# Performance work log

Hardware: AMD Instinct MI355X
Metric: run time of the kernel (lower is better)

The kernel has to match this reference:

```python
import jax, jax.numpy as jnp
import numpy as np

B, T, C, H = 4, 4096, 1024, 64

def setup_inputs() -> dict:
    key = jax.random.key(0)
    kx, kq, kk, kv = jax.random.split(key, 4)
    x = jax.random.normal(kx, (B, T, C), dtype=jnp.float32)
    scale = 1.0 / np.sqrt(C)
    Wq = jax.random.normal(kq, (C, H), dtype=jnp.float32) * scale
    Wk = jax.random.normal(kk, (C, H), dtype=jnp.float32) * scale
    Wv = jax.random.normal(kv, (C, H), dtype=jnp.float32) * scale
    return {"x": x, "Wq": Wq, "Wk": Wk, "Wv": Wv}

def reference(x, Wq, Wk, Wv):
    Bsz, Tlen, _ = x.shape
    head_size = Wq.shape[1]
    q = x @ Wq  # [B,T,H]
    k = x @ Wk
    v = x @ Wv
    # scores [B,T,T], scaled by sqrt(head_size)
    scores = jnp.einsum('bqh,bkh->bqk', q, k) / jnp.sqrt(jnp.float32(head_size))
    causal = jnp.tril(jnp.ones((Tlen, Tlen), dtype=bool))
    scores = jnp.where(causal, scores, -jnp.inf)
    weights = jax.nn.softmax(scores, axis=-1)
    # dropout p=0.0 -> identity
    return jnp.einsum('bqk,bkh->bqh', weights, v)
```

## Files before the change

### kernel.cpp

```cpp
#include <hip/hip_runtime.h>
#include <hip/hip_bf16.h>

typedef __attribute__((ext_vector_type(8))) short short8;
typedef __attribute__((ext_vector_type(4))) float f32x4;

#define MFMA16(a, b, c) __builtin_amdgcn_mfma_f32_16x16x32_bf16((a), (b), (c), 0, 0, 0)

typedef const __attribute__((address_space(1))) unsigned int* gas_t;
typedef __attribute__((address_space(3))) unsigned int* las_t;
#define GLDS16(g, l) __builtin_amdgcn_global_load_lds((gas_t)(g), (las_t)(l), 16, 0, 0)

__device__ inline unsigned short f2bf(float f) {
    union { float f; unsigned int u; } v;
    v.f = f;
    unsigned int u = v.u;
    return (unsigned short)((u + 0x7fffu + ((u >> 16) & 1u)) >> 16);
}

__device__ inline float bf2f(unsigned short u) {
    union { unsigned int u; float f; } v;
    v.u = ((unsigned int)u) << 16;
    return v.f;
}

__device__ inline size_t WF(int n, int c) {
    return ((((size_t)(n >> 4)) * 32 + (c >> 5)) * 64 + ((c >> 3) & 3) * 16 + (n & 15)) * 8 + (c & 7);
}
__device__ inline size_t QKF(int q, int h) {
    return ((((size_t)(q >> 4)) * 2 + (h >> 5)) * 64 + ((h >> 3) & 3) * 16 + (q & 15)) * 8 + (h & 7);
}
__device__ inline size_t VF(int h, int t) {
    return ((((size_t)(h >> 4)) * 128 + (t >> 5)) * 64 + ((t >> 3) & 3) * 16 + (h & 15)) * 8 + (t & 7);
}

__global__ __launch_bounds__(256) void prep_w(const float* __restrict__ Wq,
                                              const float* __restrict__ Wk,
                                              const float* __restrict__ Wv,
                                              unsigned short* __restrict__ Wt) {
    int idx = blockIdx.x * 256 + threadIdx.x;
    if (idx >= 192 * 1024) return;
    int n = idx >> 10;
    int c = idx & 1023;
    const float* W = (n < 64) ? Wq : ((n < 128) ? Wk : Wv);
    float v = W[c * 64 + (n & 63)];
    if (n < 64) v *= 0.125f;
    Wt[WF(n, c)] = f2bf(v);
}

__global__ __launch_bounds__(256, 4) void projt(const float* __restrict__ x,
                                                const unsigned short* __restrict__ Wt,
                                                unsigned short* __restrict__ Qs,
                                                unsigned short* __restrict__ Ks,
                                                unsigned short* __restrict__ Vt) {
    __shared__ __align__(16) float xbuf[2][32 * 128];

    const int tid = threadIdx.x;
    const int w = tid >> 6;
    const int lane = tid & 63;
    const int lr = lane & 15;
    const int lg = lane >> 4;
    const int t0 = blockIdx.x * 32;

    f32x4 acc[2][3];
#pragma unroll
    for (int rg = 0; rg < 2; rg++)
#pragma unroll
        for (int i = 0; i < 3; i++) acc[rg][i] = (f32x4){0.f, 0.f, 0.f, 0.f};

#define STAGE_X(buf, c0)                                                       \
    {                                                                          \
        _Pragma("unroll")                                                      \
        for (int p = 0; p < 4; p++) {                                          \
            int row = w * 8 + p * 2 + (lane >> 5);                             \
            int chunk = (lane & 31) ^ (row & 7);                               \
            const float* src = x + (size_t)(t0 + row) * 1024 + (c0) + chunk * 4;\
            float* dst = &xbuf[buf][(w * 8 + p * 2) * 128];  \
            GLDS16(src, dst);                                                  \
        }                                                                      \
    }

    STAGE_X(0, 0);
    __syncthreads();

    int cur = 0;
    for (int t = 0; t < 8; ++t) {
        if (t < 7) STAGE_X(cur ^ 1, (t + 1) * 128);

        const char* xb = (const char*)&xbuf[cur][0];
#pragma unroll
        for (int h = 0; h < 4; h++) {
            short8 bfr[3];
#pragma unroll
            for (int nt = 0; nt < 3; nt++)
                bfr[nt] = *(const short8*)(Wt +
                    (((size_t)(w * 3 + nt) * 32 + (t * 4 + h)) * 64 + lane) * 8);
            int cb = h * 8 + lg * 2;
            short8 a[2];
#pragma unroll
            for (int rg = 0; rg < 2; rg++) {
                int row = rg * 16 + lr;
                float4 a0 = *(const float4*)(xb + row * 512 + ((cb) ^ (row & 7)) * 16);
                float4 a1 = *(const float4*)(xb + row * 512 + ((cb + 1) ^ (row & 7)) * 16);
                short8 av;
                av[0] = (short)f2bf(a0.x); av[1] = (short)f2bf(a0.y);
                av[2] = (short)f2bf(a0.z); av[3] = (short)f2bf(a0.w);
                av[4] = (short)f2bf(a1.x); av[5] = (short)f2bf(a1.y);
                av[6] = (short)f2bf(a1.z); av[7] = (short)f2bf(a1.w);
                a[rg] = av;
            }
#pragma unroll
            for (int rg = 0; rg < 2; rg++)
#pragma unroll
                for (int nt = 0; nt < 3; nt++)
                    acc[rg][nt] = MFMA16(a[rg], bfr[nt], acc[rg][nt]);
        }
        __syncthreads();
        cur ^= 1;
    }

    const int nbase = w * 48;
#pragma unroll
    for (int rg = 0; rg < 2; rg++) {
#pragma unroll
        for (int nt = 0; nt < 3; nt++) {
#pragma unroll
            for (int r = 0; r < 4; r++) {
                int n = nbase + nt * 16 + lr;
                int tq = t0 + rg * 16 + lg * 4 + r;
                int b = tq >> 12;
                int qq = tq & 4095;
                unsigned short val = f2bf(acc[rg][nt][r]);
                if (n < 64) {
                    Qs[(size_t)b * 262144 + QKF(qq, n)] = val;
                } else if (n < 128) {
                    Ks[(size_t)b * 262144 + QKF(qq, n - 64)] = val;
                } else {
                    Vt[(size_t)b * 262144 + VF(n - 128, qq)] = val;
                }
            }
        }
    }
}

#define SROW 72

template <int NS>
__global__ __launch_bounds__(64) void attn(const unsigned short* __restrict__ Qs,
                                           const unsigned short* __restrict__ Ks,
                                           const unsigned short* __restrict__ Vt,
                                           float* __restrict__ out,
                                           unsigned short* __restrict__ accP,
                                           float* __restrict__ mP,
                                           float* __restrict__ lP) {
    __shared__ unsigned short pl[32 * SROW];

    const int ntasks = 512 * NS;
    int raw = ntasks - 1 - blockIdx.x;
    int qt_g = raw / NS;
    int c = raw - qt_g * NS;
    int qt = qt_g >> 2;
    int b = qt_g & 3;
    int q0 = qt * 32;

    int lane = threadIdx.x;
    int lr = lane & 15;
    int lg = lane >> 4;

    const unsigned short* Qb = Qs + (size_t)b * 262144;
    const unsigned short* Kb = Ks + (size_t)b * 262144;
    const unsigned short* Vb = Vt + (size_t)b * 262144;

    short8 qf[2][2];
#pragma unroll
    for (int qs = 0; qs < 2; qs++)
#pragma unroll
        for (int kh = 0; kh < 2; kh++)
            qf[qs][kh] = *(const short8*)(Qb +
                (((size_t)((q0 >> 4) + qs) * 2 + kh) * 64 + lane) * 8);

    f32x4 acc[4][2];
#pragma unroll
    for (int i = 0; i < 4; i++)
#pragma unroll
        for (int qs = 0; qs < 2; qs++) acc[i][qs] = (f32x4){0.f, 0.f, 0.f, 0.f};
    float m[2] = {-1e30f, -1e30f};
    float l[2] = {0.f, 0.f};

    int nt = (q0 + 95) >> 6;
    int tb = (c * nt) / NS;
    int te = ((c + 1) * nt) / NS;

    short8 kf[4][2];
    if (tb < te) {
#pragma unroll
        for (int t = 0; t < 4; t++)
#pragma unroll
            for (int half = 0; half < 2; half++)
                kf[t][half] = *(const short8*)(Kb +
                    (((size_t)((tb * 64) >> 4) + t) * 2 + half) * 512 + lane * 8);
    }

    for (int t64 = tb; t64 < te; ++t64) {
        int kv0 = t64 * 64;

        f32x4 s[4][2];
#pragma unroll
        for (int t = 0; t < 4; t++)
#pragma unroll
            for (int qs = 0; qs < 2; qs++) {
                f32x4 z = (f32x4){0.f, 0.f, 0.f, 0.f};
                z = MFMA16(kf[t][0], qf[qs][0], z);
                z = MFMA16(kf[t][1], qf[qs][1], z);
                s[t][qs] = z;
            }

        short8 vf[4][2];
#pragma unroll
        for (int ht = 0; ht < 4; ht++)
#pragma unroll
            for (int half = 0; half < 2; half++)
                vf[ht][half] = *(const short8*)(Vb +
                    (((size_t)ht * 128 + (kv0 >> 5) + half) * 64 + lane) * 8);

        if (t64 + 1 < te) {
            int kvn = (t64 + 1) * 64;
#pragma unroll
            for (int t = 0; t < 4; t++)
#pragma unroll
                for (int half = 0; half < 2; half++)
                    kf[t][half] = *(const short8*)(Kb +
                        (((size_t)(kvn >> 4) + t) * 2 + half) * 512 + lane * 8);
        }

        if (kv0 + 63 > q0) {
#pragma unroll
            for (int t = 0; t < 4; t++)
#pragma unroll
                for (int qs = 0; qs < 2; qs++)
#pragma unroll
                    for (int r = 0; r < 4; r++) {
                        int kv = kv0 + t * 16 + lg * 4 + r;
                        if (kv > q0 + qs * 16 + lr) s[t][qs][r] = -1e30f;
                    }
        }

        float pmax[2] = {-1e30f, -1e30f};
#pragma unroll
        for (int t = 0; t < 4; t++)
#pragma unroll
            for (int qs = 0; qs < 2; qs++)
#pragma unroll
                for (int r = 0; r < 4; r++) pmax[qs] = fmaxf(pmax[qs], s[t][qs][r]);

        int ok = (pmax[0] <= m[0] + 8.0f) && (pmax[1] <= m[1] + 8.0f);
        if (!__all(ok)) {
            float alpha[2];
#pragma unroll
            for (int qs = 0; qs < 2; qs++) {
                float mx = pmax[qs];
                mx = fmaxf(mx, __shfl_xor(mx, 16));
                mx = fmaxf(mx, __shfl_xor(mx, 32));
                float mn = fmaxf(m[qs], mx);
                alpha[qs] = __expf(m[qs] - mn);
                m[qs] = mn;
                l[qs] *= alpha[qs];
            }
            float ar[2][4];
#pragma unroll
            for (int qs = 0; qs < 2; qs++)
#pragma unroll
                for (int r = 0; r < 4; r++) ar[qs][r] = __shfl(alpha[qs], lg * 4 + r);
#pragma unroll
            for (int ht = 0; ht < 4; ht++)
#pragma unroll
                for (int qs = 0; qs < 2; qs++)
#pragma unroll
                    for (int r = 0; r < 4; r++) acc[ht][qs][r] *= ar[qs][r];
        }

#pragma unroll
        for (int t = 0; t < 4; t++)
#pragma unroll
            for (int qs = 0; qs < 2; qs++)
#pragma unroll
                for (int r = 0; r < 4; r++) {
                    float e = __expf(s[t][qs][r] - m[qs]);
                    s[t][qs][r] = e;
                    l[qs] += e;
                }

#pragma unroll
        for (int qs = 0; qs < 2; qs++)
#pragma unroll
            for (int t = 0; t < 4; t++) {
                uint2 uu;
                uu.x = (unsigned)f2bf(s[t][qs][0]) | ((unsigned)f2bf(s[t][qs][1]) << 16);
                uu.y = (unsigned)f2bf(s[t][qs][2]) | ((unsigned)f2bf(s[t][qs][3]) << 16);
                *(uint2*)&pl[(qs * 16 + lr) * SROW + t * 16 + lg * 4] = uu;
            }
        asm volatile("s_waitcnt lgkmcnt(0)" ::: "memory");
        __builtin_amdgcn_sched_barrier(0);
        short8 pa[2][2];
#pragma unroll
        for (int qs = 0; qs < 2; qs++)
#pragma unroll
            for (int half = 0; half < 2; half++)
                pa[qs][half] = *(const short8*)&pl[(qs * 16 + lr) * SROW +
                                                   half * 32 + lg * 8];

#pragma unroll
        for (int ht = 0; ht < 4; ht++)
#pragma unroll
            for (int qs = 0; qs < 2; qs++) {
                acc[ht][qs] = MFMA16(pa[qs][0], vf[ht][0], acc[ht][qs]);
                acc[ht][qs] = MFMA16(pa[qs][1], vf[ht][1], acc[ht][qs]);
            }
    }

    float lt[2];
#pragma unroll
    for (int qs = 0; qs < 2; qs++) {
        float v = l[qs];
        v += __shfl_xor(v, 16);
        v += __shfl_xor(v, 32);
        lt[qs] = v;
    }

    if (NS == 1) {
        float rl[2][4];
#pragma unroll
        for (int qs = 0; qs < 2; qs++)
#pragma unroll
            for (int r = 0; r < 4; r++) rl[qs][r] = 1.0f / __shfl(lt[qs], lg * 4 + r);
#pragma unroll
        for (int ht = 0; ht < 4; ht++)
#pragma unroll
            for (int qs = 0; qs < 2; qs++)
#pragma unroll
                for (int r = 0; r < 4; r++) {
                    size_t o = ((size_t)b * 4096 + q0 + qs * 16 + lg * 4 + r) * 64 +
                               ht * 16 + lr;
                    out[o] = acc[ht][qs][r] * rl[qs][r];
                }
    } else {
        int tidx = qt_g * NS + c;
        unsigned short* ap = accP + (size_t)tidx * 2048;
#pragma unroll
        for (int ht = 0; ht < 4; ht++)
#pragma unroll
            for (int qs = 0; qs < 2; qs++)
#pragma unroll
                for (int r = 0; r < 4; r++)
                    ap[(qs * 16 + lg * 4 + r) * 64 + ht * 16 + lr] =
                        f2bf(acc[ht][qs][r]);
        if (lane < 16) {
#pragma unroll
            for (int qs = 0; qs < 2; qs++) {
                mP[tidx * 32 + qs * 16 + lane] = m[qs];
                lP[tidx * 32 + qs * 16 + lane] = lt[qs];
            }
        }
    }
}

template <int NS>
__global__ __launch_bounds__(256) void combine(const unsigned short* __restrict__ accP,
                                               const float* __restrict__ mP,
                                               const float* __restrict__ lP,
                                               float* __restrict__ out) {
    int g = blockIdx.x * 256 + threadIdx.x;
    int h = g & 63;
    int row = g >> 6;
    int b = row >> 12;
    int t = row & 4095;
    int qt = t >> 5;
    int qr = t & 31;
    int qt_g = qt * 4 + b;

    float mc[NS];
    float M = -1e30f;
#pragma unroll
    for (int c = 0; c < NS; c++) {
        mc[c] = mP[(qt_g * NS + c) * 32 + qr];
        M = fmaxf(M, mc[c]);
    }
    float num = 0.f, den = 0.f;
#pragma unroll
    for (int c = 0; c < NS; c++) {
        float wgt = __expf(mc[c] - M);
        den += wgt * lP[(qt_g * NS + c) * 32 + qr];
        num += wgt * bf2f(accP[(size_t)(qt_g * NS + c) * 2048 + qr * 64 + h]);
    }
    out[g] = num / den;
}

extern "C" void kernel_launch(void* const* d_in, const int* in_sizes, int n_in,
                              void* d_out, int out_size, void* d_ws, size_t ws_size,
                              hipStream_t stream) {
    const float* x  = (const float*)d_in[0];
    const float* Wq = (const float*)d_in[1];
    const float* Wk = (const float*)d_in[2];
    const float* Wv = (const float*)d_in[3];
    float* out = (float*)d_out;

    char* ws = (char*)d_ws;
    unsigned short* Qs = (unsigned short*)(ws);
    unsigned short* Ks = (unsigned short*)(ws + (2u << 20));
    unsigned short* Vt = (unsigned short*)(ws + (4u << 20));
    unsigned short* Wt = (unsigned short*)(ws + (6u << 20));
    unsigned short* accP = (unsigned short*)(ws + (8u << 20));
    float* mP = (float*)(ws + (24u << 20));
    float* lP = (float*)(ws + (24u << 20) + (512u << 10));

    prep_w<<<768, 256, 0, stream>>>(Wq, Wk, Wv, Wt);
    projt<<<512, 256, 0, stream>>>(x, Wt, Qs, Ks, Vt);

    if (ws_size >= (25u << 20)) {
        attn<8><<<4096, 64, 0, stream>>>(Qs, Ks, Vt, out, accP, mP, lP);
        combine<8><<<4096, 256, 0, stream>>>(accP, mP, lP, out);
    } else {
        attn<1><<<512, 64, 0, stream>>>(Qs, Ks, Vt, out, accP, mP, lP);
    }
}
```

Measured before the change: 71.25 us.

## Register-prefetch x slabs in projection and halve attention KV split count

The projection kernel stops using async global-to-LDS loads. It now loads 64-column slabs of x into registers two steps ahead, writes them to a smaller double-buffered LDS tile with a new XOR swizzle, and uses a single barrier per step with a fully unrolled 16-step loop. Separately, the split-KV attention drops from 8 splits to 4, halving the attention grid and the partial results the combine kernel must merge. The trade-offs are more registers and less parallelism in attention.

```diff
diff --git a/kernel.cpp b/kernel.cpp
--- a/kernel.cpp
+++ b/kernel.cpp
@@ -5,10 +5,6 @@
 typedef __attribute__((ext_vector_type(4))) float f32x4;
 
 #define MFMA16(a, b, c) __builtin_amdgcn_mfma_f32_16x16x32_bf16((a), (b), (c), 0, 0, 0)
-
-typedef const __attribute__((address_space(1))) unsigned int* gas_t;
-typedef __attribute__((address_space(3))) unsigned int* las_t;
-#define GLDS16(g, l) __builtin_amdgcn_global_load_lds((gas_t)(g), (las_t)(l), 16, 0, 0)
 
 __device__ inline unsigned short f2bf(float f) {
     union { float f; unsigned int u; } v;
@@ -52,7 +48,7 @@
                                                 unsigned short* __restrict__ Qs,
                                                 unsigned short* __restrict__ Ks,
                                                 unsigned short* __restrict__ Vt) {
-    __shared__ __align__(16) float xbuf[2][32 * 128];
+    __shared__ __align__(16) float xbuf[2][32 * 64];
 
     const int tid = threadIdx.x;
     const int w = tid >> 6;
@@ -61,46 +57,65 @@
     const int lg = lane >> 4;
     const int t0 = blockIdx.x * 32;
 
-    f32x4 acc[2][3];
-#pragma unroll
-    for (int rg = 0; rg < 2; rg++)
-#pragma unroll
-        for (int i = 0; i < 3; i++) acc[rg][i] = (f32x4){0.f, 0.f, 0.f, 0.f};
-
-#define STAGE_X(buf, c0)                                                       \
+    const int sr0 = w * 8 + (lane >> 4);
+    const int sch = lane & 15;
+
+#define LOADSLAB(v, sl)                                                        \
+    {                                                                          \
+        const uint4* xr = (const uint4*)(x + (size_t)(t0) * 1024 + (sl) * 64); \
+        v[0] = xr[(size_t)(sr0) * 256 + sch];                                  \
+        v[1] = xr[(size_t)(sr0 + 4) * 256 + sch];                              \
+    }
+
+#define DSWRITE(buf, v)                                                        \
     {                                                                          \
         _Pragma("unroll")                                                      \
-        for (int p = 0; p < 4; p++) {                                          \
-            int row = w * 8 + p * 2 + (lane >> 5);                             \
-            int chunk = (lane & 31) ^ (row & 7);                               \
-            const float* src = x + (size_t)(t0 + row) * 1024 + (c0) + chunk * 4;\
-            float* dst = &xbuf[buf][(w * 8 + p * 2) * 128];  \
-            GLDS16(src, dst);                                                  \
+        for (int j = 0; j < 2; j++) {                                          \
+            int row = sr0 + j * 4;                                             \
+            int l = sch ^ (row & 15);                                          \
+            *(uint4*)&xbuf[buf][row * 64 + l * 4] = v[j];                      \
         }                                                                      \
     }
 
-    STAGE_X(0, 0);
-    __syncthreads();
-
-    int cur = 0;
-    for (int t = 0; t < 8; ++t) {
-        if (t < 7) STAGE_X(cur ^ 1, (t + 1) * 128);
-
-        const char* xb = (const char*)&xbuf[cur][0];
-#pragma unroll
-        for (int h = 0; h < 4; h++) {
+    uint4 vc[2], vn[2];
+    LOADSLAB(vc, 0);
+    DSWRITE(0, vc);
+    LOADSLAB(vc, 1);
+
+    f32x4 acc[2][3];
+#pragma unroll
+    for (int rg = 0; rg < 2; rg++)
+#pragma unroll
+        for (int i = 0; i < 3; i++) acc[rg][i] = (f32x4){0.f, 0.f, 0.f, 0.f};
+
+#pragma unroll
+    for (int t = 0; t < 16; ++t) {
+        if (t + 2 < 16) LOADSLAB(vn, t + 2);
+
+        asm volatile("s_waitcnt lgkmcnt(0)" ::: "memory");
+        __builtin_amdgcn_sched_barrier(0);
+        __builtin_amdgcn_s_barrier();
+        __builtin_amdgcn_sched_barrier(0);
+
+        if (t + 1 < 16) DSWRITE((t + 1) & 1, vc);
+
+        const float* xb = &xbuf[t & 1][0];
+#pragma unroll
+        for (int h = 0; h < 2; h++) {
             short8 bfr[3];
 #pragma unroll
             for (int nt = 0; nt < 3; nt++)
                 bfr[nt] = *(const short8*)(Wt +
-                    (((size_t)(w * 3 + nt) * 32 + (t * 4 + h)) * 64 + lane) * 8);
+                    (((size_t)(w * 3 + nt) * 32 + (t * 2 + h)) * 64 + lane) * 8);
             int cb = h * 8 + lg * 2;
+            int l0 = cb ^ lr;
+            int l1 = (cb + 1) ^ lr;
             short8 a[2];
 #pragma unroll
             for (int rg = 0; rg < 2; rg++) {
                 int row = rg * 16 + lr;
-                float4 a0 = *(const float4*)(xb + row * 512 + ((cb) ^ (row & 7)) * 16);
-                float4 a1 = *(const float4*)(xb + row * 512 + ((cb + 1) ^ (row & 7)) * 16);
+                float4 a0 = *(const float4*)&xb[row * 64 + l0 * 4];
+                float4 a1 = *(const float4*)&xb[row * 64 + l1 * 4];
                 short8 av;
                 av[0] = (short)f2bf(a0.x); av[1] = (short)f2bf(a0.y);
                 av[2] = (short)f2bf(a0.z); av[3] = (short)f2bf(a0.w);
@@ -114,8 +129,8 @@
                 for (int nt = 0; nt < 3; nt++)
                     acc[rg][nt] = MFMA16(a[rg], bfr[nt], acc[rg][nt]);
         }
-        __syncthreads();
-        cur ^= 1;
+
+        if (t + 2 < 16) { vc[0] = vn[0]; vc[1] = vn[1]; }
     }
 
     const int nbase = w * 48;
@@ -416,8 +431,8 @@
     projt<<<512, 256, 0, stream>>>(x, Wt, Qs, Ks, Vt);
 
     if (ws_size >= (25u << 20)) {
-        attn<8><<<4096, 64, 0, stream>>>(Qs, Ks, Vt, out, accP, mP, lP);
-        combine<8><<<4096, 256, 0, stream>>>(accP, mP, lP, out);
+        attn<4><<<2048, 64, 0, stream>>>(Qs, Ks, Vt, out, accP, mP, lP);
+        combine<4><<<4096, 256, 0, stream>>>(accP, mP, lP, out);
     } else {
         attn<1><<<512, 64, 0, stream>>>(Qs, Ks, Vt, out, accP, mP, lP);
     }
```

New measurement: 61.45 us (median of 2 runs). 1.16x faster.
